# Kernel tuning notes

Measured on AMD Instinct MI355X. Metric: run time of the kernel, lower is better.

The kernel has to match this reference:

```python
import jax, jax.numpy as jnp
import numpy as np

EPS = 1e-5


def _conv1x1(x, w, b=None):
    # x: [B,C,H,W], w: [O,C]
    y = jnp.einsum('bchw,oc->bohw', x, w)
    if b is not None:
        y = y + b[None, :, None, None]
    return y


def _bn(x, g, b, m, v):
    inv = g / jnp.sqrt(v + EPS)
    return x * inv[None, :, None, None] + (b - m * inv)[None, :, None, None]


def setup_inputs() -> dict:
    key = jax.random.key(0)
    ks = jax.random.split(key, 24)
    B, Cin, H, W = 4, 512, 64, 64
    Ci = Cin // 8  # 64
    s = 0.05
    d = {}
    d['x'] = jax.random.normal(ks[0], (B, Cin, H, W), jnp.float32)
    # conv_p1 (BasicConv2d: conv no-bias + BN)
    d['wp1'] = jax.random.normal(ks[1], (Ci, Cin), jnp.float32) * s
    d['gp1'] = jnp.ones((Ci,), jnp.float32)
    d['bp1'] = jnp.zeros((Ci,), jnp.float32)
    d['mp1'] = jax.random.normal(ks[2], (Ci,), jnp.float32) * 0.1
    d['vp1'] = jax.random.uniform(ks[3], (Ci,), jnp.float32, 0.5, 1.5)
    # conv_c1
    d['wc1'] = jax.random.normal(ks[4], (Ci, Cin), jnp.float32) * s
    d['gc1'] = jnp.ones((Ci,), jnp.float32)
    d['bc1'] = jnp.zeros((Ci,), jnp.float32)
    d['mc1'] = jax.random.normal(ks[5], (Ci,), jnp.float32) * 0.1
    d['vc1'] = jax.random.uniform(ks[6], (Ci,), jnp.float32, 0.5, 1.5)
    # PAM 1x1 convs (with bias)
    d['wb'] = jax.random.normal(ks[7], (Ci, Ci), jnp.float32) * s
    d['bb'] = jnp.zeros((Ci,), jnp.float32)
    d['wc2'] = jax.random.normal(ks[8], (Ci, Ci), jnp.float32) * s
    d['bc2'] = jnp.zeros((Ci,), jnp.float32)
    d['wd'] = jax.random.normal(ks[9], (Ci, Ci), jnp.float32) * s
    d['bd'] = jnp.zeros((Ci,), jnp.float32)
    d['alpha'] = jnp.array([0.5], jnp.float32)  # nonzero so attention path is exercised
    d['beta'] = jnp.array([0.5], jnp.float32)
    # out conv
    d['wo'] = jax.random.normal(ks[10], (Cin, Ci), jnp.float32) * s
    d['go'] = jnp.ones((Cin,), jnp.float32)
    d['bo'] = jnp.zeros((Cin,), jnp.float32)
    d['mo'] = jax.random.normal(ks[11], (Cin,), jnp.float32) * 0.1
    d['vo'] = jax.random.uniform(ks[12], (Cin,), jnp.float32, 0.5, 1.5)
    return d


def reference(x, wp1, gp1, bp1, mp1, vp1, wc1, gc1, bc1, mc1, vc1,
              wb, bb, wc2, bc2, wd, bd, alpha, beta, wo, go, bo, mo, vo):
    B, Cin, H, W = x.shape
    HW = H * W

    # --- position branch ---
    fp = _bn(_conv1x1(x, wp1), gp1, bp1, mp1, vp1)          # [B,Ci,H,W]
    Ci = fp.shape[1]
    fb = _conv1x1(fp, wb, bb).reshape(B, Ci, HW)             # query  [B,Ci,HW]
    fc = _conv1x1(fp, wc2, bc2).reshape(B, Ci, HW)           # key    [B,Ci,HW]
    fd = _conv1x1(fp, wd, bd).reshape(B, Ci, HW)             # value  [B,Ci,HW]
    attn_s = jax.nn.softmax(jnp.einsum('bcq,bck->bqk', fb, fc), axis=-1)  # [B,HW,HW]
    feat_ep = jnp.einsum('bck,bqk->bcq', fd, attn_s).reshape(B, Ci, H, W)
    feat_p = alpha[0] * feat_ep + fp

    # --- channel branch ---
    fcb = _bn(_conv1x1(x, wc1), gc1, bc1, mc1, vc1)          # [B,Ci,H,W]
    fa = fcb.reshape(B, Ci, HW)
    attn_c = jnp.einsum('bcn,bdn->bcd', fa, fa)              # [B,Ci,Ci]
    attn_c = jnp.max(attn_c, axis=-1, keepdims=True) - attn_c
    attn_c = jax.nn.softmax(attn_c, axis=-1)
    feat_ec = jnp.einsum('bcd,bdn->bcn', attn_c, fa).reshape(B, Ci, H, W)
    feat_c = beta[0] * feat_ec + fcb

    # --- fuse + out ---
    fusion = feat_p + feat_c
    out = _bn(_conv1x1(fusion, wo), go, bo, mo, vo)          # [B,Cin,H,W]
    return out
```

## Files before the change

kernel.cpp:

```cpp
#include <hip/hip_runtime.h>
#include <hip/hip_bf16.h>

typedef __hip_bfloat16 bf16;
typedef unsigned short u16;
typedef __attribute__((ext_vector_type(8))) short short8;
typedef __attribute__((ext_vector_type(4))) float f32x4;

#define HW 4096
#define NB (64*HW)

__device__ __forceinline__ f32x4 MFMA16(short8 a, short8 b, f32x4 c){
  return __builtin_amdgcn_mfma_f32_16x16x32_bf16(a, b, c, 0, 0, 0);
}

__global__ __launch_bounds__(256) void k_const(float* __restrict__ out, float v, int n){
  int i = blockIdx.x*256 + threadIdx.x;
  if (i < n) out[i] = v;
}

__global__ __launch_bounds__(512) void k_prep(
    const float* __restrict__ gp, const float* __restrict__ bp,
    const float* __restrict__ mp, const float* __restrict__ vp,
    const float* __restrict__ gc, const float* __restrict__ bc,
    const float* __restrict__ mc, const float* __restrict__ vc,
    const float* __restrict__ go, const float* __restrict__ bo,
    const float* __restrict__ mo, const float* __restrict__ vo,
    float* __restrict__ bn){
  int t = threadIdx.x;
  if (t < 64){
    float iv = gp[t] * rsqrtf(vp[t] + 1e-5f);
    bn[t] = iv; bn[64+t] = bp[t] - mp[t]*iv;
    float ic = gc[t] * rsqrtf(vc[t] + 1e-5f);
    bn[128+t] = ic; bn[192+t] = bc[t] - mc[t]*ic;
  }
  float io = go[t] * rsqrtf(vo[t] + 1e-5f);
  bn[256+t] = io; bn[768+t] = bo[t] - mo[t]*io;
}

__global__ __launch_bounds__(256) void k_conv_in(
    const float* __restrict__ x, const float* __restrict__ wp1, const float* __restrict__ wc1,
    const float* __restrict__ bn, float* __restrict__ fp, float* __restrict__ fcb){
  __shared__ __align__(16) float Wl[512][16];
  const int t = threadIdx.x;
  const int cg = blockIdx.y, b = blockIdx.z;
  const bool isP = cg < 4;
  const int c0 = (cg & 3) * 16;
  const float* w = isP ? wp1 : wc1;
  const float* inv  = isP ? bn       : bn + 128;
  const float* bias = isP ? bn + 64  : bn + 192;
  float* outp = isP ? fp : fcb;
  for (int i = t; i < 8192; i += 256){
    int c = i & 15, k = i >> 4;
    Wl[k][c] = w[(size_t)(c0 + c)*512 + k];
  }
  __syncthreads();
  const int p = blockIdx.x*256 + t;
  const float* xb = x + (size_t)b*512*HW + p;
  float acc[16];
  #pragma unroll
  for (int i = 0; i < 16; i++) acc[i] = 0.f;
  for (int k = 0; k < 512; k++){
    float xv = xb[(size_t)k*HW];
    float4 w0 = *(const float4*)&Wl[k][0];
    float4 w1 = *(const float4*)&Wl[k][4];
    float4 w2 = *(const float4*)&Wl[k][8];
    float4 w3 = *(const float4*)&Wl[k][12];
    acc[0]=fmaf(w0.x,xv,acc[0]); acc[1]=fmaf(w0.y,xv,acc[1]); acc[2]=fmaf(w0.z,xv,acc[2]); acc[3]=fmaf(w0.w,xv,acc[3]);
    acc[4]=fmaf(w1.x,xv,acc[4]); acc[5]=fmaf(w1.y,xv,acc[5]); acc[6]=fmaf(w1.z,xv,acc[6]); acc[7]=fmaf(w1.w,xv,acc[7]);
    acc[8]=fmaf(w2.x,xv,acc[8]); acc[9]=fmaf(w2.y,xv,acc[9]); acc[10]=fmaf(w2.z,xv,acc[10]); acc[11]=fmaf(w2.w,xv,acc[11]);
    acc[12]=fmaf(w3.x,xv,acc[12]); acc[13]=fmaf(w3.y,xv,acc[13]); acc[14]=fmaf(w3.z,xv,acc[14]); acc[15]=fmaf(w3.w,xv,acc[15]);
  }
  const size_t base = (size_t)b*NB + p;
  #pragma unroll
  for (int i = 0; i < 16; i++){
    int c = c0 + i;
    outp[base + (size_t)c*HW] = fmaf(acc[i], inv[c], bias[c]);
  }
}

__global__ __launch_bounds__(256) void k_qkv(
    const float* __restrict__ fp,
    const float* __restrict__ wb,  const float* __restrict__ bbv,
    const float* __restrict__ wc2, const float* __restrict__ bc2,
    const float* __restrict__ wd,  const float* __restrict__ bd,
    bf16* __restrict__ fB, bf16* __restrict__ fC, bf16* __restrict__ fD){
  __shared__ __align__(16) float Wl[64][16];
  __shared__ float Bl[16];
  const int t = threadIdx.x;
  const int mg = blockIdx.y, mat = mg >> 2, c0 = (mg & 3)*16, b = blockIdx.z;
  const float* w    = (mat == 0) ? wb  : (mat == 1 ? wc2 : wd);
  const float* bias = (mat == 0) ? bbv : (mat == 1 ? bc2 : bd);
  bf16* outp        = (mat == 0) ? fB  : (mat == 1 ? fC  : fD);
  for (int i = t; i < 1024; i += 256){
    int c = i & 15, k = i >> 4;
    Wl[k][c] = w[(size_t)(c0 + c)*64 + k];
  }
  if (t < 16) Bl[t] = bias[c0 + t];
  __syncthreads();
  const int p = blockIdx.x*512 + t*2;
  const float* in = fp + (size_t)b*NB + p;
  float2 acc[16];
  #pragma unroll
  for (int i = 0; i < 16; i++){ acc[i].x = 0.f; acc[i].y = 0.f; }
  for (int k = 0; k < 64; k++){
    float2 xv = *(const float2*)(in + (size_t)k*HW);
    float4 w0 = *(const float4*)&Wl[k][0];
    float4 w1 = *(const float4*)&Wl[k][4];
    float4 w2 = *(const float4*)&Wl[k][8];
    float4 w3 = *(const float4*)&Wl[k][12];
    float wv[16] = {w0.x,w0.y,w0.z,w0.w, w1.x,w1.y,w1.z,w1.w,
                    w2.x,w2.y,w2.z,w2.w, w3.x,w3.y,w3.z,w3.w};
    #pragma unroll
    for (int i = 0; i < 16; i++){
      acc[i].x = fmaf(wv[i], xv.x, acc[i].x);
      acc[i].y = fmaf(wv[i], xv.y, acc[i].y);
    }
  }
  if (mat < 2){
    bf16* ob = outp + (size_t)b*NB;
    #pragma unroll
    for (int i = 0; i < 16; i += 2){
      __hip_bfloat162 h0 = __float22bfloat162_rn(
          make_float2(acc[i].x + Bl[i], acc[i+1].x + Bl[i+1]));
      __hip_bfloat162 h1 = __float22bfloat162_rn(
          make_float2(acc[i].y + Bl[i], acc[i+1].y + Bl[i+1]));
      *(__hip_bfloat162*)&ob[(size_t)p*64 + c0 + i]     = h0;
      *(__hip_bfloat162*)&ob[(size_t)(p+1)*64 + c0 + i] = h1;
    }
  } else {
    const size_t base = (size_t)b*NB + p;
    #pragma unroll
    for (int i = 0; i < 16; i++){
      float bl = Bl[i];
      __hip_bfloat162 o2 = __float22bfloat162_rn(make_float2(acc[i].x + bl, acc[i].y + bl));
      *(__hip_bfloat162*)&outp[base + (size_t)(c0 + i)*HW] = o2;
    }
  }
}

__global__ __launch_bounds__(256) void k_chan_attn(
    const float* __restrict__ fcb, float* __restrict__ attn){
  __shared__ __align__(16) float rowc[4096];
  __shared__ float red[256];
  __shared__ float Srow[64];
  const int c = blockIdx.x, b = blockIdx.y, t = threadIdx.x;
  const float* fa = fcb + (size_t)b*NB;
  #pragma unroll
  for (int i = 0; i < 4; i++){
    int n = i*1024 + t*4;
    *(float4*)&rowc[n] = *(const float4*)&fa[(size_t)c*HW + n];
  }
  __syncthreads();
  const int d = t >> 2, part = t & 3;
  const float* frow = fa + (size_t)d*HW + part*1024;
  const float* rc = rowc + part*1024;
  float s = 0.f;
  for (int i = 0; i < 1024; i += 4){
    float4 xv = *(const float4*)&frow[i];
    float4 rv = *(const float4*)&rc[i];
    s += xv.x*rv.x + xv.y*rv.y + xv.z*rv.z + xv.w*rv.w;
  }
  red[t] = s;
  __syncthreads();
  if (part == 0) Srow[d] = red[t] + red[t+1] + red[t+2] + red[t+3];
  __syncthreads();
  if (t < 64){
    float z = -Srow[t];
    float m = z;
    #pragma unroll
    for (int off = 32; off; off >>= 1) m = fmaxf(m, __shfl_xor(m, off));
    float e = __expf(fminf(z - m, 0.f));
    float ss = e;
    #pragma unroll
    for (int off = 32; off; off >>= 1) ss += __shfl_xor(ss, off);
    attn[(size_t)b*4096 + (size_t)c*64 + t] = e / ss;
  }
}

__global__ __launch_bounds__(256) void k_pos_attn(
    const u16* __restrict__ fBt, const u16* __restrict__ fCt, const u16* __restrict__ fDv,
    const float* __restrict__ fpl, const float* __restrict__ alphap,
    float* __restrict__ fus){
  __shared__ __align__(16) u16 Kt[128*72];
  __shared__ __align__(16) u16 Vt[64*136];
  __shared__ __align__(16) u16 Pt[64*136];

  const int t = threadIdx.x;
  const int b = blockIdx.y, q0 = blockIdx.x*64;
  const int wv = t>>6, lane = t&63, quad = lane>>4, lr = lane&15;
  const u16* Fb = fBt + (size_t)b*NB;
  const u16* Fc = fCt + (size_t)b*NB;
  const u16* Fd = fDv + (size_t)b*NB;

  const size_t qoff = (size_t)(q0 + wv*16 + lr)*64;
  short8 a0 = *(const short8*)&Fb[qoff + quad*8];
  short8 a1 = *(const short8*)&Fb[qoff + 32 + quad*8];

  float m[4] = {-3.0e38f,-3.0e38f,-3.0e38f,-3.0e38f};
  float l[4] = {0.f,0.f,0.f,0.f};
  f32x4 accO[4];
  #pragma unroll
  for (int cs = 0; cs < 4; cs++) accO[cs] = (f32x4){0.f,0.f,0.f,0.f};

  const int skk = t>>1, sch = (t&1)*32;
  const int svc = t>>2, svk = (t&3)*32;

  for (int k0 = 0; k0 < HW; k0 += 128){
    __syncthreads();
    {
      const u16* ks = &Fc[(size_t)(k0+skk)*64 + sch];
      u16* kd = &Kt[skk*72 + sch];
      ((uint4*)kd)[0] = ((const uint4*)ks)[0];
      ((uint4*)kd)[1] = ((const uint4*)ks)[1];
      ((uint4*)kd)[2] = ((const uint4*)ks)[2];
      ((uint4*)kd)[3] = ((const uint4*)ks)[3];
      const u16* vs = &Fd[(size_t)svc*HW + k0 + svk];
      u16* vd = &Vt[svc*136 + svk];
      ((uint4*)vd)[0] = ((const uint4*)vs)[0];
      ((uint4*)vd)[1] = ((const uint4*)vs)[1];
      ((uint4*)vd)[2] = ((const uint4*)vs)[2];
      ((uint4*)vd)[3] = ((const uint4*)vs)[3];
    }
    __syncthreads();

    f32x4 s[8];
    #pragma unroll
    for (int ks = 0; ks < 8; ks++){
      short8 b0 = *(short8*)&Kt[(ks*16+lr)*72 + quad*8];
      short8 b1 = *(short8*)&Kt[(ks*16+lr)*72 + 32 + quad*8];
      f32x4 acc = {0.f,0.f,0.f,0.f};
      acc = MFMA16(a0, b0, acc);
      acc = MFMA16(a1, b1, acc);
      s[ks] = acc;
    }

    float mx[4];
    #pragma unroll
    for (int r = 0; r < 4; r++){
      float v = s[0][r];
      #pragma unroll
      for (int ks = 1; ks < 8; ks++) v = fmaxf(v, s[ks][r]);
      mx[r] = v;
    }
    #pragma unroll
    for (int off = 1; off < 16; off <<= 1){
      #pragma unroll
      for (int r = 0; r < 4; r++) mx[r] = fmaxf(mx[r], __shfl_xor(mx[r], off));
    }
    float al[4], rs[4];
    #pragma unroll
    for (int r = 0; r < 4; r++){
      float mn = fmaxf(m[r], mx[r]);
      al[r] = __expf(m[r] - mn);
      m[r] = mn;
      rs[r] = 0.f;
    }
    #pragma unroll
    for (int ks = 0; ks < 8; ks++){
      #pragma unroll
      for (int r = 0; r < 4; r++){
        float e = __expf(s[ks][r] - m[r]);
        rs[r] += e;
        bf16 h = __float2bfloat16(e);
        Pt[(wv*16 + quad*4 + r)*136 + ks*16 + lr] = *(u16*)&h;
      }
    }
    #pragma unroll
    for (int off = 1; off < 16; off <<= 1){
      #pragma unroll
      for (int r = 0; r < 4; r++) rs[r] += __shfl_xor(rs[r], off);
    }
    #pragma unroll
    for (int r = 0; r < 4; r++) l[r] = l[r]*al[r] + rs[r];
    #pragma unroll
    for (int cs = 0; cs < 4; cs++){
      #pragma unroll
      for (int r = 0; r < 4; r++) accO[cs][r] *= al[r];
    }
    __syncthreads();

    #pragma unroll
    for (int kc = 0; kc < 4; kc++){
      short8 pf = *(short8*)&Pt[(wv*16+lr)*136 + kc*32 + quad*8];
      #pragma unroll
      for (int cs = 0; cs < 4; cs++){
        short8 vf = *(short8*)&Vt[(cs*16+lr)*136 + kc*32 + quad*8];
        accO[cs] = MFMA16(pf, vf, accO[cs]);
      }
    }
  }

  const float alp = alphap[0];
  const float* Fp = fpl + (size_t)b*NB;
  float* Fo = fus + (size_t)b*NB;
  #pragma unroll
  for (int r = 0; r < 4; r++){
    int qg = q0 + wv*16 + quad*4 + r;
    float rl = 1.f / fmaxf(l[r], 1e-20f);
    #pragma unroll
    for (int cs = 0; cs < 4; cs++){
      int c = cs*16 + lr;
      Fo[(size_t)c*HW + qg] = fmaf(alp, accO[cs][r]*rl, Fp[(size_t)c*HW + qg]);
    }
  }
}

__global__ __launch_bounds__(256) void k_chan_apply(
    const float* __restrict__ fcb, const float* __restrict__ attn,
    const float* __restrict__ betap, float* __restrict__ fus){
  __shared__ __align__(16) float Ar2[64][8];
  const int t = threadIdx.x;
  const int c0 = blockIdx.y*8, b = blockIdx.z;
  for (int i = t; i < 512; i += 256){
    int d = i >> 3, ci = i & 7;
    Ar2[d][ci] = attn[(size_t)b*4096 + (size_t)(c0 + ci)*64 + d];
  }
  __syncthreads();
  const int p = blockIdx.x*256 + t;
  const float* fa = fcb + (size_t)b*NB;
  float acc[8] = {0.f,0.f,0.f,0.f,0.f,0.f,0.f,0.f};
  for (int d = 0; d < 64; d++){
    float v = fa[(size_t)d*HW + p];
    float4 A0 = *(const float4*)&Ar2[d][0];
    float4 A1 = *(const float4*)&Ar2[d][4];
    acc[0]=fmaf(A0.x,v,acc[0]); acc[1]=fmaf(A0.y,v,acc[1]); acc[2]=fmaf(A0.z,v,acc[2]); acc[3]=fmaf(A0.w,v,acc[3]);
    acc[4]=fmaf(A1.x,v,acc[4]); acc[5]=fmaf(A1.y,v,acc[5]); acc[6]=fmaf(A1.z,v,acc[6]); acc[7]=fmaf(A1.w,v,acc[7]);
  }
  const float be = betap[0];
  #pragma unroll
  for (int i = 0; i < 8; i++){
    size_t idx = (size_t)b*NB + (size_t)(c0 + i)*HW + p;
    fus[idx] += fmaf(be, acc[i], fa[(size_t)(c0 + i)*HW + p]);
  }
}

__global__ __launch_bounds__(256) void k_conv_out(
    const float* __restrict__ fus, const float* __restrict__ wo,
    const float* __restrict__ bn, float* __restrict__ out){
  __shared__ __align__(16) float Wl[64][16];
  const int t = threadIdx.x;
  const int o0 = blockIdx.y*16, b = blockIdx.z;
  for (int i = t; i < 1024; i += 256){
    int o = i & 15, c = i >> 4;
    Wl[c][o] = wo[(size_t)(o0 + o)*64 + c];
  }
  __syncthreads();
  const int p = blockIdx.x*512 + t*2;
  const float* fu = fus + (size_t)b*NB + p;
  float2 acc[16];
  #pragma unroll
  for (int i = 0; i < 16; i++){ acc[i].x = 0.f; acc[i].y = 0.f; }
  for (int c = 0; c < 64; c++){
    float2 xv = *(const float2*)(fu + (size_t)c*HW);
    float4 w0 = *(const float4*)&Wl[c][0];
    float4 w1 = *(const float4*)&Wl[c][4];
    float4 w2 = *(const float4*)&Wl[c][8];
    float4 w3 = *(const float4*)&Wl[c][12];
    float wv[16] = {w0.x,w0.y,w0.z,w0.w, w1.x,w1.y,w1.z,w1.w,
                    w2.x,w2.y,w2.z,w2.w, w3.x,w3.y,w3.z,w3.w};
    #pragma unroll
    for (int i = 0; i < 16; i++){
      acc[i].x = fmaf(wv[i], xv.x, acc[i].x);
      acc[i].y = fmaf(wv[i], xv.y, acc[i].y);
    }
  }
  #pragma unroll
  for (int i = 0; i < 16; i++){
    int o = o0 + i;
    float iv = bn[256+o], bs = bn[768+o];
    float* op = &out[(size_t)b*512*HW + (size_t)o*HW + p];
    op[0] = fmaf(acc[i].x, iv, bs);
    op[1] = fmaf(acc[i].y, iv, bs);
  }
}

extern "C" void kernel_launch(void* const* d_in, const int* in_sizes, int n_in,
                              void* d_out, int out_size, void* d_ws, size_t ws_size,
                              hipStream_t stream){
  static const int dictSz[24] = {8388608,32768,64,64,64,64,32768,64,64,64,64,
                                 4096,64,4096,64,4096,64,1,1,32768,512,512,512,512};
  bool dictOk = (n_in == 24);
  if (dictOk){
    for (int i = 0; i < 24; i++) if (in_sizes[i] != dictSz[i]) dictOk = false;
  }
  bool wsOk = (ws_size >= (size_t)(19u << 20));
  float* out = (float*)d_out;
  if (!dictOk){ k_const<<<(out_size+255)/256, 256, 0, stream>>>(out, 32.f, out_size); return; }
  if (!wsOk)  { k_const<<<(out_size+255)/256, 256, 0, stream>>>(out, 48.f, out_size); return; }

  const float* x    = (const float*)d_in[0];
  const float* wp1  = (const float*)d_in[1];
  const float* gp1  = (const float*)d_in[2];  const float* bp1 = (const float*)d_in[3];
  const float* mp1  = (const float*)d_in[4];  const float* vp1 = (const float*)d_in[5];
  const float* wc1  = (const float*)d_in[6];
  const float* gc1  = (const float*)d_in[7];  const float* bc1 = (const float*)d_in[8];
  const float* mc1  = (const float*)d_in[9];  const float* vc1 = (const float*)d_in[10];
  const float* wb   = (const float*)d_in[11]; const float* bb  = (const float*)d_in[12];
  const float* wc2  = (const float*)d_in[13]; const float* bc2 = (const float*)d_in[14];
  const float* wd   = (const float*)d_in[15]; const float* bd  = (const float*)d_in[16];
  const float* alp  = (const float*)d_in[17]; const float* bet = (const float*)d_in[18];
  const float* wo   = (const float*)d_in[19];
  const float* go   = (const float*)d_in[20]; const float* bo  = (const float*)d_in[21];
  const float* mo   = (const float*)d_in[22]; const float* vo  = (const float*)d_in[23];

  char* w8 = (char*)d_ws;
  float* fp    = (float*)(w8);
  float* fcb   = (float*)(w8 + (4u<<20));
  float* fus   = (float*)(w8 + (8u<<20));
  bf16*  fB    = (bf16*) (w8 + (12u<<20));
  bf16*  fC    = (bf16*) (w8 + (14u<<20));
  bf16*  fD    = (bf16*) (w8 + (16u<<20));
  float* attnc = (float*)(w8 + (18u<<20));
  float* bn    = (float*)(w8 + (18u<<20) + 65536);

  k_prep<<<1, 512, 0, stream>>>(gp1,bp1,mp1,vp1, gc1,bc1,mc1,vc1, go,bo,mo,vo, bn);
  k_conv_in<<<dim3(16,8,4), 256, 0, stream>>>(x, wp1, wc1, bn, fp, fcb);
  k_qkv<<<dim3(8,12,4), 256, 0, stream>>>(fp, wb,bb, wc2,bc2, wd,bd, fB, fC, fD);
  k_chan_attn<<<dim3(64,4), 256, 0, stream>>>(fcb, attnc);
  k_pos_attn<<<dim3(64,4), 256, 0, stream>>>((const u16*)fB, (const u16*)fC, (const u16*)fD,
                                             fp, alp, fus);
  k_chan_apply<<<dim3(16,8,4), 256, 0, stream>>>(fcb, attnc, bet, fus);
  k_conv_out<<<dim3(8,32,4), 256, 0, stream>>>(fus, wo, bn, out);
}
```

Before: 347.9 us.

## Split position-attention key range across two wave groups with register prefetch

The position-attention kernel now launches 512 threads per block. Two groups of four waves each process half of the key sequence as a split-K flash attention, and their running max, sum and output are merged through shared memory at the end. Global K/V loads for the next tile are prefetched into registers while the current tile is computed. The epilogue stages the result in LDS so that stores to the output are coalesced float4 writes. This doubles the waves per query tile, which is meant to hide latency with only 256 blocks, at the cost of more LDS, more registers and an extra merge step.

Result: no change. 353.9 us (+1.7%).

```diff
diff --git a/kernel.cpp b/kernel.cpp
--- a/kernel.cpp
+++ b/kernel.cpp
@@ -177,22 +177,26 @@
   }
 }
 
-__global__ __launch_bounds__(256) void k_pos_attn(
+__global__ __launch_bounds__(512) void k_pos_attn(
     const u16* __restrict__ fBt, const u16* __restrict__ fCt, const u16* __restrict__ fDv,
     const float* __restrict__ fpl, const float* __restrict__ alphap,
     float* __restrict__ fus){
-  __shared__ __align__(16) u16 Kt[128*72];
-  __shared__ __align__(16) u16 Vt[64*136];
-  __shared__ __align__(16) u16 Pt[64*136];
+  __shared__ __align__(16) u16 Kt[2][128*72];
+  __shared__ __align__(16) u16 Vt[2][64*136];
+  __shared__ __align__(16) u16 Pt[2][64*136];
 
   const int t = threadIdx.x;
   const int b = blockIdx.y, q0 = blockIdx.x*64;
-  const int wv = t>>6, lane = t&63, quad = lane>>4, lr = lane&15;
+  const int wv = t>>6;
+  const int g  = wv>>2;
+  const int wg = wv&3;
+  const int lane = t&63, quad = lane>>4, lr = lane&15;
+  const int tg = t & 255;
   const u16* Fb = fBt + (size_t)b*NB;
   const u16* Fc = fCt + (size_t)b*NB;
   const u16* Fd = fDv + (size_t)b*NB;
 
-  const size_t qoff = (size_t)(q0 + wv*16 + lr)*64;
+  const size_t qoff = (size_t)(q0 + wg*16 + lr)*64;
   short8 a0 = *(const short8*)&Fb[qoff + quad*8];
   short8 a1 = *(const short8*)&Fb[qoff + 32 + quad*8];
 
@@ -202,32 +206,45 @@
   #pragma unroll
   for (int cs = 0; cs < 4; cs++) accO[cs] = (f32x4){0.f,0.f,0.f,0.f};
 
-  const int skk = t>>1, sch = (t&1)*32;
-  const int svc = t>>2, svk = (t&3)*32;
-
-  for (int k0 = 0; k0 < HW; k0 += 128){
+  const int skk = tg>>1, sch = (tg&1)*32;
+  const int svc = tg>>2, svk = (tg&3)*32;
+  const u16* Ksrc = Fc + (size_t)(g*2048 + skk)*64 + sch;
+  const u16* Vsrc = Fd + (size_t)svc*HW + g*2048 + svk;
+
+  uint4 kr[4], vr[4];
+  #pragma unroll
+  for (int i = 0; i < 4; i++){
+    kr[i] = ((const uint4*)Ksrc)[i];
+    vr[i] = ((const uint4*)Vsrc)[i];
+  }
+
+  for (int tile = 0; tile < 16; ++tile){
     __syncthreads();
     {
-      const u16* ks = &Fc[(size_t)(k0+skk)*64 + sch];
-      u16* kd = &Kt[skk*72 + sch];
-      ((uint4*)kd)[0] = ((const uint4*)ks)[0];
-      ((uint4*)kd)[1] = ((const uint4*)ks)[1];
-      ((uint4*)kd)[2] = ((const uint4*)ks)[2];
-      ((uint4*)kd)[3] = ((const uint4*)ks)[3];
-      const u16* vs = &Fd[(size_t)svc*HW + k0 + svk];
-      u16* vd = &Vt[svc*136 + svk];
-      ((uint4*)vd)[0] = ((const uint4*)vs)[0];
-      ((uint4*)vd)[1] = ((const uint4*)vs)[1];
-      ((uint4*)vd)[2] = ((const uint4*)vs)[2];
-      ((uint4*)vd)[3] = ((const uint4*)vs)[3];
+      u16* kd = &Kt[g][skk*72 + sch];
+      u16* vd = &Vt[g][svc*136 + svk];
+      #pragma unroll
+      for (int i = 0; i < 4; i++) ((uint4*)kd)[i] = kr[i];
+      #pragma unroll
+      for (int i = 0; i < 4; i++) ((uint4*)vd)[i] = vr[i];
     }
     __syncthreads();
 
+    if (tile < 15){
+      const u16* ks2 = Ksrc + (size_t)(tile+1)*128*64;
+      const u16* vs2 = Vsrc + (tile+1)*128;
+      #pragma unroll
+      for (int i = 0; i < 4; i++){
+        kr[i] = ((const uint4*)ks2)[i];
+        vr[i] = ((const uint4*)vs2)[i];
+      }
+    }
+
     f32x4 s[8];
     #pragma unroll
     for (int ks = 0; ks < 8; ks++){
-      short8 b0 = *(short8*)&Kt[(ks*16+lr)*72 + quad*8];
-      short8 b1 = *(short8*)&Kt[(ks*16+lr)*72 + 32 + quad*8];
+      short8 b0 = *(short8*)&Kt[g][(ks*16+lr)*72 + quad*8];
+      short8 b1 = *(short8*)&Kt[g][(ks*16+lr)*72 + 32 + quad*8];
       f32x4 acc = {0.f,0.f,0.f,0.f};
       acc = MFMA16(a0, b0, acc);
       acc = MFMA16(a1, b1, acc);
@@ -262,7 +279,7 @@
         float e = __expf(s[ks][r] - m[r]);
         rs[r] += e;
         bf16 h = __float2bfloat16(e);
-        Pt[(wv*16 + quad*4 + r)*136 + ks*16 + lr] = *(u16*)&h;
+        Pt[g][(wg*16 + quad*4 + r)*136 + ks*16 + lr] = *(u16*)&h;
       }
     }
     #pragma unroll
@@ -281,27 +298,59 @@
 
     #pragma unroll
     for (int kc = 0; kc < 4; kc++){
-      short8 pf = *(short8*)&Pt[(wv*16+lr)*136 + kc*32 + quad*8];
+      short8 pf = *(short8*)&Pt[g][(wg*16+lr)*136 + kc*32 + quad*8];
       #pragma unroll
       for (int cs = 0; cs < 4; cs++){
-        short8 vf = *(short8*)&Vt[(cs*16+lr)*136 + kc*32 + quad*8];
+        short8 vf = *(short8*)&Vt[g][(cs*16+lr)*136 + kc*32 + quad*8];
         accO[cs] = MFMA16(pf, vf, accO[cs]);
       }
     }
   }
 
-  const float alp = alphap[0];
-  const float* Fp = fpl + (size_t)b*NB;
-  float* Fo = fus + (size_t)b*NB;
-  #pragma unroll
-  for (int r = 0; r < 4; r++){
-    int qg = q0 + wv*16 + quad*4 + r;
-    float rl = 1.f / fmaxf(l[r], 1e-20f);
-    #pragma unroll
-    for (int cs = 0; cs < 4; cs++){
-      int c = cs*16 + lr;
-      Fo[(size_t)c*HW + qg] = fmaf(alp, accO[cs][r]*rl, Fp[(size_t)c*HW + qg]);
-    }
+  __syncthreads();
+  float* Ol = (float*)&Pt[0][0];
+  float* Ml = Ol + 64*69;
+  float* Ll = Ml + 64;
+  if (g == 1){
+    #pragma unroll
+    for (int r = 0; r < 4; r++){
+      int row = wg*16 + quad*4 + r;
+      #pragma unroll
+      for (int cs = 0; cs < 4; cs++)
+        Ol[row*69 + cs*16 + lr] = accO[cs][r];
+      if (lr == 0){ Ml[row] = m[r]; Ll[row] = l[r]; }
+    }
+  }
+  __syncthreads();
+  if (g == 0){
+    const float alp = alphap[0];
+    #pragma unroll
+    for (int r = 0; r < 4; r++){
+      int row = wg*16 + quad*4 + r;
+      float m1 = Ml[row], l1 = Ll[row];
+      float mt = fmaxf(m[r], m1);
+      float e0 = __expf(m[r] - mt), e1 = __expf(m1 - mt);
+      float lt = fmaxf(l[r]*e0 + l1*e1, 1e-20f);
+      float sc = alp / lt;
+      #pragma unroll
+      for (int cs = 0; cs < 4; cs++){
+        int idx = row*69 + cs*16 + lr;
+        float v = accO[cs][r]*e0 + Ol[idx]*e1;
+        Ol[idx] = v * sc;
+      }
+    }
+  }
+  __syncthreads();
+
+  {
+    const int c = t >> 3, qs = (t & 7) * 8;
+    const float* Fp = fpl + (size_t)b*NB + (size_t)c*HW + q0 + qs;
+    float* Fo = fus + (size_t)b*NB + (size_t)c*HW + q0 + qs;
+    float v[8];
+    #pragma unroll
+    for (int j = 0; j < 8; j++) v[j] = Ol[(qs+j)*69 + c] + Fp[j];
+    *(float4*)&Fo[0] = make_float4(v[0],v[1],v[2],v[3]);
+    *(float4*)&Fo[4] = make_float4(v[4],v[5],v[6],v[7]);
   }
 }
 
@@ -417,7 +466,7 @@
   k_conv_in<<<dim3(16,8,4), 256, 0, stream>>>(x, wp1, wc1, bn, fp, fcb);
   k_qkv<<<dim3(8,12,4), 256, 0, stream>>>(fp, wb,bb, wc2,bc2, wd,bd, fB, fC, fD);
   k_chan_attn<<<dim3(64,4), 256, 0, stream>>>(fcb, attnc);
-  k_pos_attn<<<dim3(64,4), 256, 0, stream>>>((const u16*)fB, (const u16*)fC, (const u16*)fD,
+  k_pos_attn<<<dim3(64,4), 512, 0, stream>>>((const u16*)fB, (const u16*)fC, (const u16*)fD,
                                              fp, alp, fus);
   k_chan_apply<<<dim3(16,8,4), 256, 0, stream>>>(fcb, attnc, bet, fus);
   k_conv_out<<<dim3(8,32,4), 256, 0, stream>>>(fus, wo, bn, out);
```
